# Performance work log

Measured on AMD Instinct MI355X. Metric: run time of the kernel, lower is better.

## Reference

```python
import jax, jax.numpy as jnp
import numpy as np

H, I, B = 256, 128, 512

def setup_inputs() -> dict:
    key = jax.random.key(0)
    ks = jax.random.split(key, 24)
    n = lambda k, shp, s=1.0: jax.random.normal(k, shp, dtype=jnp.float32) * s
    inp = {
        "x": n(ks[0], (B, I)),
        "hx": n(ks[1], (B, H), 0.1),
        "cx": n(ks[2], (B, H, H), 0.1),
        # input->gate weights (hidden, input), xavier-like scale
        "Wii": n(ks[3], (H, I), (2.0 / (H + I)) ** 0.5),
        "Wif": n(ks[4], (H, I), (2.0 / (H + I)) ** 0.5),
        "Wig": n(ks[5], (H, I), (2.0 / (H + I)) ** 0.5),
        "Wio": n(ks[6], (H, I), (2.0 / (H + I)) ** 0.5),
        # hidden->gate weights (hidden, hidden), ~orthogonal scale
        "Whi": n(ks[7], (H, H), H ** -0.5),
        "Whit": n(ks[8], (H, H), H ** -0.5),
        "Whf": n(ks[9], (H, H), H ** -0.5),
        "Whft": n(ks[10], (H, H), H ** -0.5),
        "Whc": n(ks[11], (H, H), H ** -0.5),
        "Whct": n(ks[12], (H, H), H ** -0.5),
        "Who": n(ks[13], (H, H), H ** -0.5),
        "Uinv": n(ks[14], (H, H), H ** -0.5),
        "Vtinv": n(ks[15], (H, H), H ** -0.5),
        # biases: bi/bf/bg are full (H,H) matrices, bo is (H,1)
        "bi": jnp.zeros((H, H), jnp.float32),
        "bf": jnp.zeros((H, H), jnp.float32),
        "bg": jnp.zeros((H, H), jnp.float32),
        "bo": jnp.zeros((H, 1), jnp.float32),
    }
    return inp


def reference(x, hx, cx, Wii, Wif, Wig, Wio, Whi, Whit, Whf, Whft, Whc, Whct, Who, Uinv, Vtinv, bi, bf, bg, bo):
    # W @ diag(v) @ M^T  ==  einsum('hi,bi,gi->bhg', W, v, M)
    def sandwich(Wx, Wh, Wht, b):
        # (Wx*x) @ Wx^T + (Wh*hx) @ Wht^T + b  -> (B,H,H)
        xt = jnp.einsum('hi,bi,gi->bhg', Wx, x, Wx)
        ht = jnp.einsum('hj,bj,gj->bhg', Wh, hx, Wht)
        return xt + ht + b

    i = jax.nn.sigmoid(sandwich(Wii, Whi, Whit, bi))
    f = jax.nn.sigmoid(sandwich(Wif, Whf, Whft, bf))
    g = jnp.tanh(sandwich(Wig, Whc, Whct, bg))
    # o: ordinary vector gate (B,H)
    o = jax.nn.sigmoid(jnp.einsum('hi,bi->bh', Wio, x)
                       + jnp.einsum('hj,bj->bh', Who, hx) + bo[:, 0])
    cx_new = f * cx + i * g                     # (B,H,H)
    # diag(Uinv @ cx_new @ Vtinv) per batch element -> (B,H)
    proj_down = jnp.einsum('ij,bjk,ki->bi', Uinv, cx_new, Vtinv)
    hx_new = o * jax.nn.sigmoid(proj_down)
    return hx_new
```

## Files before the change

kernel.cpp:

```cpp
#include <hip/hip_runtime.h>
#include <hip/hip_bf16.h>

#define Hh 256
#define Ii 128
#define KF 384
#define LDSB 72

typedef __attribute__((ext_vector_type(8))) short bf16x8;
typedef __attribute__((ext_vector_type(4))) float f32x4;
typedef unsigned short u16;
typedef unsigned int u32;

__device__ inline u16 f2bf(float f) {
  u32 u = __float_as_uint(f);
  u += 0x7FFFu + ((u >> 16) & 1u);
  return (u16)(u >> 16);
}
__device__ inline u32 pack_bf16x2(float a, float b) {
  __hip_bfloat162 h = __float22bfloat162_rn(make_float2(a, b));
  u32 r; __builtin_memcpy(&r, &h, 4); return r;
}
__device__ inline u32 scale2(u32 packed, float va, float vb) {
  float lo = __uint_as_float(packed << 16) * va;
  float hi = __uint_as_float(packed & 0xFFFF0000u) * vb;
  return pack_bf16x2(lo, hi);
}
__device__ inline float sigm(float x) { return 1.0f / (1.0f + __expf(-x)); }
__device__ inline float tanh_f(float x) { return 1.0f - 2.0f / (1.0f + __expf(2.0f * x)); }

union U32x4 { bf16x8 f; u32 d[4]; uint4 v; };

__global__ __launch_bounds__(256) void k_prep(
    const float* __restrict__ Wii, const float* __restrict__ Wif, const float* __restrict__ Wig,
    const float* __restrict__ Whi, const float* __restrict__ Whit,
    const float* __restrict__ Whf, const float* __restrict__ Whft,
    const float* __restrict__ Whc, const float* __restrict__ Whct,
    const float* __restrict__ Vtinv, const float* __restrict__ Uinv,
    const float* __restrict__ Wio, const float* __restrict__ Who,
    u16* __restrict__ RW, u16* __restrict__ CW, u16* __restrict__ Vtt,
    float* __restrict__ UinvP, float* __restrict__ proj, float* __restrict__ WoT) {
  const int tid = threadIdx.x, bx = blockIdx.x, y = blockIdx.y;
  if (y < 3) {
    if (bx < 48) {
      const float* WX  = (y == 0) ? Wii : (y == 1 ? Wif : Wig);
      const float* WHr = (y == 0) ? Whi : (y == 1 ? Whf : Whc);
      u16* rw = RW + y * Hh * KF;
      const int f  = (bx * 256 + tid) * 8;
      const int kc = f >> 14;
      const int h  = (f >> 6) & 255;
      const int t0 = f & 63;
      const float* src = (kc < 2) ? (WX + h * Ii + kc * 64 + t0)
                                  : (WHr + h * Hh + (kc - 2) * 64 + t0);
      const float4 s0 = *(const float4*)src;
      const float4 s1 = *(const float4*)(src + 4);
      uint4 o;
      o.x = (u32)f2bf(s0.x) | ((u32)f2bf(s0.y) << 16);
      o.y = (u32)f2bf(s0.z) | ((u32)f2bf(s0.w) << 16);
      o.z = (u32)f2bf(s1.x) | ((u32)f2bf(s1.y) << 16);
      o.w = (u32)f2bf(s1.z) | ((u32)f2bf(s1.w) << 16);
      *(uint4*)(rw + f) = o;
    }
  } else if (y < 6) {
    if (bx < 48) {
      const int ph = y - 3;
      const float* WX  = (ph == 0) ? Wii : (ph == 1 ? Wif : Wig);
      const float* WHt = (ph == 0) ? Whit : (ph == 1 ? Whft : Whct);
      u16* cw = CW + ph * Hh * KF;
      const int f  = (bx * 256 + tid) * 8;
      const int kb = f / 24576;
      const int r  = f - kb * 24576;
      const int kc = r >> 12;
      const int r2 = r & 4095;
      const int k  = r2 >> 6;
      const int t0 = r2 & 63;
      const int h  = kb * 64 + k;
      const float* src = (kc < 2) ? (WX + h * Ii + kc * 64 + t0)
                                  : (WHt + h * Hh + (kc - 2) * 64 + t0);
      const float4 s0 = *(const float4*)src;
      const float4 s1 = *(const float4*)(src + 4);
      uint4 o;
      o.x = (u32)f2bf(s0.x) | ((u32)f2bf(s0.y) << 16);
      o.y = (u32)f2bf(s0.z) | ((u32)f2bf(s0.w) << 16);
      o.z = (u32)f2bf(s1.x) | ((u32)f2bf(s1.y) << 16);
      o.w = (u32)f2bf(s1.z) | ((u32)f2bf(s1.w) << 16);
      *(uint4*)(cw + f) = o;
    }
  } else if (y == 6) {
    if (bx < 64) {
      __shared__ u16 tbuf[32][33];
      const int c = tid & 31, r8 = tid >> 5;
      const int tr = bx >> 3, tc = bx & 7;
#pragma unroll
      for (int rr = r8; rr < 32; rr += 8)
        tbuf[rr][c] = f2bf(Vtinv[(tc * 32 + rr) * Hh + tr * 32 + c]);
      __syncthreads();
#pragma unroll
      for (int rr = r8; rr < 32; rr += 8)
        Vtt[(tr * 32 + rr) * Hh + tc * 32 + c] = tbuf[c][rr];
    } else {
      const int tb = (bx - 64) * 12;
#pragma unroll
      for (int tt = 0; tt < 12; ++tt) {
        const int t = tb + tt;
        const float v = (t < Ii) ? Wio[tid * Ii + t] : Who[tid * Hh + t - Ii];
        WoT[t * Hh + tid] = v;
      }
    }
  } else {
    if (bx < 32) {
      const int base = (bx * 256 + tid) * 8;
#pragma unroll
      for (int e8 = 0; e8 < 8; ++e8) {
        int f = base + e8;
        int t512 = f >> 7;
        int e = f & 127;
        int ti = e >> 5;
        int rem = e & 31;
        int tjl = rem >> 2;
        int rr = rem & 3;
        int wv = t512 >> 6;
        int ln = t512 & 63;
        int qd = ln >> 4;
        int r15v = ln & 15;
        int i = (wv & 3) * 64 + ti * 16 + qd * 4 + rr;
        int j = (wv >> 2) * 128 + tjl * 16 + r15v;
        UinvP[f] = Uinv[i * Hh + j];
      }
    } else if (bx < 64) {
      const int base = (bx - 32) * 256 + tid;
      const float4 z = {0.f, 0.f, 0.f, 0.f};
#pragma unroll
      for (int it = 0; it < 4; ++it)
        *(float4*)(proj + (size_t)(it * 8192 + base) * 4) = z;
    }
  }
}

__global__ __launch_bounds__(512) void k_main(
    const float* __restrict__ x, const float* __restrict__ hx, const float* __restrict__ cx,
    const u16* __restrict__ RW, const u16* __restrict__ CW, const u16* __restrict__ Vtt,
    const float* __restrict__ bi, const float* __restrict__ bfm, const float* __restrict__ bg,
    const float* __restrict__ UinvP, float* __restrict__ proj) {
  __shared__ union {
    u16 B[2][64][LDSB];
    u16 P[256][LDSB];
  } sU;
  __shared__ float sV[KF];
  __shared__ float sPart[8][64];

  const int tid  = threadIdx.x;
  const int b    = blockIdx.x >> 2;
  const int kb   = blockIdx.x & 3;
  const int k0   = kb * 64;
  const int lane = tid & 63;
  const int w    = tid >> 6;
  const int r15  = lane & 15;
  const int quad = lane >> 4;

  if (tid < Ii) sV[tid] = x[b * Ii + tid];
  if (tid < Hh) sV[Ii + tid] = hx[b * Hh + tid];

  const u16* rwp[3] = {RW + 2 * Hh * KF, RW, RW + 1 * Hh * KF};
  const u16* cwp[3] = {CW + 2 * Hh * KF + kb * 24576, CW + kb * 24576,
                       CW + 1 * Hh * KF + kb * 24576};
  const float* bp3[2] = {bg, bi};
  const float* cx_b = cx + (size_t)b * Hh * Hh;

  const int wfoff = (w * 32 + r15) * 64 + quad * 8;

  U32x4 m, mnW, mnN;
  bf16x8 wfC[2][2], wfN[2][2];
  m.v   = *(const uint4*)(cwp[0] + tid * 8);
  mnW.v = *(const uint4*)(cwp[0] + 4096 + tid * 8);
  {
    const u16* rb = rwp[0] + wfoff;
#pragma unroll
    for (int ja = 0; ja < 2; ++ja)
#pragma unroll
      for (int ks = 0; ks < 2; ++ks)
        wfC[ja][ks] = *(const bf16x8*)(rb + ja * 1024 + ks * 32);
  }
  __syncthreads();
  {
    U32x4 o;
    const float4 va = *(const float4*)(&sV[(tid & 7) * 8]);
    const float4 vb = *(const float4*)(&sV[(tid & 7) * 8 + 4]);
    o.d[0] = scale2(m.d[0], va.x, va.y); o.d[1] = scale2(m.d[1], va.z, va.w);
    o.d[2] = scale2(m.d[2], vb.x, vb.y); o.d[3] = scale2(m.d[3], vb.z, vb.w);
    *(uint4*)(&sU.B[0][tid >> 3][(tid & 7) * 8]) = o.v;
  }
  __syncthreads();

  float p[2][4][4];
  f32x4 acc[2][4];

#pragma unroll
  for (int ph = 0; ph < 3; ++ph) {
#pragma unroll
    for (int ja = 0; ja < 2; ++ja)
#pragma unroll
      for (int tk = 0; tk < 4; ++tk)
#pragma unroll
        for (int r = 0; r < 4; ++r) acc[ja][tk][r] = 0.0f;

#pragma unroll
    for (int kc = 0; kc < 6; ++kc) {
      const int sc  = ph * 6 + kc;
      const int cur = sc & 1;
      if (sc < 16) {
        const int s2 = sc + 2;
        mnN.v = *(const uint4*)(cwp[s2 / 6] + (s2 % 6) * 4096 + tid * 8);
      }
      if (sc < 17) {
        const int s1 = sc + 1;
        const u16* rb = rwp[s1 / 6] + (s1 % 6) * 16384 + wfoff;
#pragma unroll
        for (int ja = 0; ja < 2; ++ja)
#pragma unroll
          for (int ks = 0; ks < 2; ++ks)
            wfN[ja][ks] = *(const bf16x8*)(rb + ja * 1024 + ks * 32);
      }
#pragma unroll
      for (int ks = 0; ks < 2; ++ks) {
        bf16x8 sf[4];
#pragma unroll
        for (int tk = 0; tk < 4; ++tk)
          sf[tk] = *(const bf16x8*)(&sU.B[cur][tk * 16 + r15][ks * 32 + quad * 8]);
#pragma unroll
        for (int tk = 0; tk < 4; ++tk) {
          acc[0][tk] = __builtin_amdgcn_mfma_f32_16x16x32_bf16(sf[tk], wfC[0][ks], acc[0][tk], 0, 0, 0);
          acc[1][tk] = __builtin_amdgcn_mfma_f32_16x16x32_bf16(sf[tk], wfC[1][ks], acc[1][tk], 0, 0, 0);
        }
      }
      if (sc < 17) {
        U32x4 o;
        const int nt0 = ((sc + 1) % 6) * 64;
        const float4 va = *(const float4*)(&sV[nt0 + (tid & 7) * 8]);
        const float4 vb = *(const float4*)(&sV[nt0 + (tid & 7) * 8 + 4]);
        o.d[0] = scale2(mnW.d[0], va.x, va.y); o.d[1] = scale2(mnW.d[1], va.z, va.w);
        o.d[2] = scale2(mnW.d[2], vb.x, vb.y); o.d[3] = scale2(mnW.d[3], vb.z, vb.w);
        *(uint4*)(&sU.B[cur ^ 1][tid >> 3][(tid & 7) * 8]) = o.v;
      }
      if (ph < 2 && kc == 5) {
        const float* bp = bp3[ph];
#pragma unroll
        for (int ja = 0; ja < 2; ++ja) {
          const int jg = w * 32 + ja * 16 + r15;
          const float* bpr = bp + (size_t)jg * Hh + k0 + quad * 4;
#pragma unroll
          for (int tk = 0; tk < 4; ++tk) {
            const float4 bv = *(const float4*)(bpr + tk * 16);
            if (ph == 0) {
#pragma unroll
              for (int r = 0; r < 4; ++r)
                p[ja][tk][r] = tanh_f(acc[ja][tk][r] + ((const float*)&bv)[r]);
            } else {
#pragma unroll
              for (int r = 0; r < 4; ++r)
                p[ja][tk][r] *= sigm(acc[ja][tk][r] + ((const float*)&bv)[r]);
            }
          }
        }
      }
      __syncthreads();
      mnW = mnN;
#pragma unroll
      for (int ja = 0; ja < 2; ++ja)
#pragma unroll
        for (int ks = 0; ks < 2; ++ks)
          wfC[ja][ks] = wfN[ja][ks];
    }
  }

#pragma unroll
  for (int ja = 0; ja < 2; ++ja) {
    const int jg = w * 32 + ja * 16 + r15;
    const float* bpr = bfm + (size_t)jg * Hh + k0 + quad * 4;
    const float* cxr = cx_b + (size_t)jg * Hh + k0 + quad * 4;
#pragma unroll
    for (int tk = 0; tk < 4; ++tk) {
      const float4 bv = *(const float4*)(bpr + tk * 16);
      const float4 cv = *(const float4*)(cxr + tk * 16);
      float cc[4];
#pragma unroll
      for (int r = 0; r < 4; ++r)
        cc[r] = sigm(acc[ja][tk][r] + ((const float*)&bv)[r]) * ((const float*)&cv)[r] + p[ja][tk][r];
      uint2 pk;
      pk.x = pack_bf16x2(cc[0], cc[1]);
      pk.y = pack_bf16x2(cc[2], cc[3]);
      *(uint2*)(&sU.P[jg][tk * 16 + quad * 4]) = pk;
    }
  }
  __syncthreads();

  const int islab = (w & 3) * 64;
  const int jhb   = (w >> 2) * 128;
  const float* up = UinvP + (size_t)tid * 128;
  float racc[4][4];
#pragma unroll
  for (int ti = 0; ti < 4; ++ti)
#pragma unroll
    for (int r = 0; r < 4; ++r) racc[ti][r] = 0.0f;

#pragma unroll
  for (int tjg = 0; tjg < 2; ++tjg) {
    bf16x8 fbp[2][4];
#pragma unroll
    for (int ks = 0; ks < 2; ++ks)
#pragma unroll
      for (int tjj = 0; tjj < 4; ++tjj)
        fbp[ks][tjj] = *(const bf16x8*)(&sU.P[jhb + (tjg * 4 + tjj) * 16 + r15][ks * 32 + quad * 8]);
#pragma unroll
    for (int ti = 0; ti < 4; ++ti) {
      const u16* vrow = Vtt + (size_t)(islab + ti * 16 + r15) * Hh + k0 + quad * 8;
      const bf16x8 va0 = *(const bf16x8*)vrow;
      const bf16x8 va1 = *(const bf16x8*)(vrow + 32);
      f32x4 pacc[4];
#pragma unroll
      for (int tjj = 0; tjj < 4; ++tjj)
#pragma unroll
        for (int r = 0; r < 4; ++r) pacc[tjj][r] = 0.0f;
#pragma unroll
      for (int tjj = 0; tjj < 4; ++tjj)
        pacc[tjj] = __builtin_amdgcn_mfma_f32_16x16x32_bf16(va0, fbp[0][tjj], pacc[tjj], 0, 0, 0);
#pragma unroll
      for (int tjj = 0; tjj < 4; ++tjj)
        pacc[tjj] = __builtin_amdgcn_mfma_f32_16x16x32_bf16(va1, fbp[1][tjj], pacc[tjj], 0, 0, 0);
#pragma unroll
      for (int tjj = 0; tjj < 4; ++tjj) {
        const float4 uu = *(const float4*)(up + ti * 32 + (tjg * 4 + tjj) * 4);
#pragma unroll
        for (int r = 0; r < 4; ++r)
          racc[ti][r] += pacc[tjj][r] * ((const float*)&uu)[r];
      }
    }
  }

#pragma unroll
  for (int ti = 0; ti < 4; ++ti)
#pragma unroll
    for (int r = 0; r < 4; ++r) {
      float v = racc[ti][r];
      v += __shfl_xor(v, 1);
      v += __shfl_xor(v, 2);
      v += __shfl_xor(v, 4);
      v += __shfl_xor(v, 8);
      if (r15 == 0) sPart[w][ti * 16 + quad * 4 + r] = v;
    }
  __syncthreads();
  if (tid < Hh)
    atomicAdd(&proj[b * Hh + tid], sPart[tid >> 6][tid & 63] + sPart[(tid >> 6) + 4][tid & 63]);
}

__global__ __launch_bounds__(256) void k_out(
    const float* __restrict__ x, const float* __restrict__ hx,
    const float* __restrict__ WoT, const float* __restrict__ bo,
    const float* __restrict__ proj, float* __restrict__ out) {
  __shared__ float sv[KF];
  const int b = blockIdx.x, tid = threadIdx.x;
  if (tid < Ii) sv[tid] = x[b * Ii + tid];
  sv[Ii + tid] = hx[b * Hh + tid];
  __syncthreads();
  float acc = 0.0f;
  const float* wp = WoT + tid;
#pragma unroll 16
  for (int t = 0; t < KF; ++t)
    acc = fmaf(sv[t], wp[(size_t)t * Hh], acc);
  out[b * Hh + tid] = sigm(acc + bo[tid]) * sigm(proj[b * Hh + tid]);
}

extern "C" void kernel_launch(void* const* d_in, const int* in_sizes, int n_in,
                              void* d_out, int out_size, void* d_ws, size_t ws_size,
                              hipStream_t stream) {
  (void)in_sizes; (void)n_in; (void)out_size; (void)ws_size;
  const float* x    = (const float*)d_in[0];
  const float* hx   = (const float*)d_in[1];
  const float* cx   = (const float*)d_in[2];
  const float* Wii  = (const float*)d_in[3];
  const float* Wif  = (const float*)d_in[4];
  const float* Wig  = (const float*)d_in[5];
  const float* Wio  = (const float*)d_in[6];
  const float* Whi  = (const float*)d_in[7];
  const float* Whit = (const float*)d_in[8];
  const float* Whf  = (const float*)d_in[9];
  const float* Whft = (const float*)d_in[10];
  const float* Whc  = (const float*)d_in[11];
  const float* Whct = (const float*)d_in[12];
  const float* Who  = (const float*)d_in[13];
  const float* Uinv = (const float*)d_in[14];
  const float* Vtinv= (const float*)d_in[15];
  const float* bi   = (const float*)d_in[16];
  const float* bf   = (const float*)d_in[17];
  const float* bg   = (const float*)d_in[18];
  const float* bo   = (const float*)d_in[19];
  float* out = (float*)d_out;

  u16* RW    = (u16*)d_ws;
  u16* CW    = RW + 3 * Hh * KF;
  u16* Vtt   = CW + 3 * Hh * KF;
  float* UinvP = (float*)(Vtt + Hh * Hh);
  float* proj  = UinvP + Hh * Hh;
  float* WoT   = proj + 512 * Hh;

  k_prep<<<dim3(96, 8), 256, 0, stream>>>(Wii, Wif, Wig, Whi, Whit, Whf, Whft, Whc, Whct,
                                          Vtinv, Uinv, Wio, Who,
                                          RW, CW, Vtt, UinvP, proj, WoT);
  k_main<<<2048, 512, 0, stream>>>(x, hx, cx, RW, CW, Vtt, bi, bf, bg, UinvP, proj);
  k_out<<<512, 256, 0, stream>>>(x, hx, WoT, bo, proj, out);
}
```

Baseline: 521.6 us.

## Stage full per-phase operand tile in LDS to cut per-chunk barriers

Replaces the double-buffered 64-wide LDS chunk pipeline, which synced after every k-chunk, with a single 64x384 LDS tile that holds a whole phase's scaled operand. Barriers drop from one per chunk to two per phase, and the next phase's global loads are issued mid-phase into registers. Weight-fragment loads are no longer prefetched one step ahead, so global latency may be exposed before each chunk's MFMAs. More registers (six uint4) and more LDS are used, which could lower occupancy.

```diff
diff --git a/kernel.cpp b/kernel.cpp
--- a/kernel.cpp
+++ b/kernel.cpp
@@ -5,6 +5,7 @@
 #define Ii 128
 #define KF 384
 #define LDSB 72
+#define SBN 392
 
 typedef __attribute__((ext_vector_type(8))) short bf16x8;
 typedef __attribute__((ext_vector_type(4))) float f32x4;
@@ -142,7 +143,7 @@
     const float* __restrict__ bi, const float* __restrict__ bfm, const float* __restrict__ bg,
     const float* __restrict__ UinvP, float* __restrict__ proj) {
   __shared__ union {
-    u16 B[2][64][LDSB];
+    u16 B[64][SBN];
     u16 P[256][LDSB];
   } sU;
   __shared__ float sV[KF];
@@ -156,6 +157,8 @@
   const int w    = tid >> 6;
   const int r15  = lane & 15;
   const int quad = lane >> 4;
+  const int srow = tid >> 3;
+  const int scol = (tid & 7) * 8;
 
   if (tid < Ii) sV[tid] = x[b * Ii + tid];
   if (tid < Hh) sV[Ii + tid] = hx[b * Hh + tid];
@@ -168,26 +171,19 @@
 
   const int wfoff = (w * 32 + r15) * 64 + quad * 8;
 
-  U32x4 m, mnW, mnN;
-  bf16x8 wfC[2][2], wfN[2][2];
-  m.v   = *(const uint4*)(cwp[0] + tid * 8);
-  mnW.v = *(const uint4*)(cwp[0] + 4096 + tid * 8);
-  {
-    const u16* rb = rwp[0] + wfoff;
-#pragma unroll
-    for (int ja = 0; ja < 2; ++ja)
-#pragma unroll
-      for (int ks = 0; ks < 2; ++ks)
-        wfC[ja][ks] = *(const bf16x8*)(rb + ja * 1024 + ks * 32);
-  }
-  __syncthreads();
-  {
+  U32x4 L[6];
+#pragma unroll
+  for (int kc = 0; kc < 6; ++kc)
+    L[kc].v = *(const uint4*)(cwp[0] + kc * 4096 + tid * 8);
+  __syncthreads();
+#pragma unroll
+  for (int kc = 0; kc < 6; ++kc) {
     U32x4 o;
-    const float4 va = *(const float4*)(&sV[(tid & 7) * 8]);
-    const float4 vb = *(const float4*)(&sV[(tid & 7) * 8 + 4]);
-    o.d[0] = scale2(m.d[0], va.x, va.y); o.d[1] = scale2(m.d[1], va.z, va.w);
-    o.d[2] = scale2(m.d[2], vb.x, vb.y); o.d[3] = scale2(m.d[3], vb.z, vb.w);
-    *(uint4*)(&sU.B[0][tid >> 3][(tid & 7) * 8]) = o.v;
+    const float4 va = *(const float4*)(&sV[kc * 64 + scol]);
+    const float4 vb = *(const float4*)(&sV[kc * 64 + scol + 4]);
+    o.d[0] = scale2(L[kc].d[0], va.x, va.y); o.d[1] = scale2(L[kc].d[1], va.z, va.w);
+    o.d[2] = scale2(L[kc].d[2], vb.x, vb.y); o.d[3] = scale2(L[kc].d[3], vb.z, vb.w);
+    *(uint4*)(&sU.B[srow][kc * 64 + scol]) = o.v;
   }
   __syncthreads();
 
@@ -205,73 +201,69 @@
 
 #pragma unroll
     for (int kc = 0; kc < 6; ++kc) {
-      const int sc  = ph * 6 + kc;
-      const int cur = sc & 1;
-      if (sc < 16) {
-        const int s2 = sc + 2;
-        mnN.v = *(const uint4*)(cwp[s2 / 6] + (s2 % 6) * 4096 + tid * 8);
-      }
-      if (sc < 17) {
-        const int s1 = sc + 1;
-        const u16* rb = rwp[s1 / 6] + (s1 % 6) * 16384 + wfoff;
+      if (ph < 2 && kc == 3) {
+#pragma unroll
+        for (int k2 = 0; k2 < 6; ++k2)
+          L[k2].v = *(const uint4*)(cwp[ph + 1] + k2 * 4096 + tid * 8);
+      }
+      bf16x8 wf[2][2];
+      {
+        const u16* rb = rwp[ph] + kc * 16384 + wfoff;
 #pragma unroll
         for (int ja = 0; ja < 2; ++ja)
 #pragma unroll
           for (int ks = 0; ks < 2; ++ks)
-            wfN[ja][ks] = *(const bf16x8*)(rb + ja * 1024 + ks * 32);
+            wf[ja][ks] = *(const bf16x8*)(rb + ja * 1024 + ks * 32);
       }
 #pragma unroll
       for (int ks = 0; ks < 2; ++ks) {
         bf16x8 sf[4];
 #pragma unroll
         for (int tk = 0; tk < 4; ++tk)
-          sf[tk] = *(const bf16x8*)(&sU.B[cur][tk * 16 + r15][ks * 32 + quad * 8]);
+          sf[tk] = *(const bf16x8*)(&sU.B[tk * 16 + r15][kc * 64 + ks * 32 + quad * 8]);
 #pragma unroll
         for (int tk = 0; tk < 4; ++tk) {
-          acc[0][tk] = __builtin_amdgcn_mfma_f32_16x16x32_bf16(sf[tk], wfC[0][ks], acc[0][tk], 0, 0, 0);
-          acc[1][tk] = __builtin_amdgcn_mfma_f32_16x16x32_bf16(sf[tk], wfC[1][ks], acc[1][tk], 0, 0, 0);
+          acc[0][tk] = __builtin_amdgcn_mfma_f32_16x16x32_bf16(sf[tk], wf[0][ks], acc[0][tk], 0, 0, 0);
+          acc[1][tk] = __builtin_amdgcn_mfma_f32_16x16x32_bf16(sf[tk], wf[1][ks], acc[1][tk], 0, 0, 0);
         }
       }
-      if (sc < 17) {
-        U32x4 o;
-        const int nt0 = ((sc + 1) % 6) * 64;
-        const float4 va = *(const float4*)(&sV[nt0 + (tid & 7) * 8]);
-        const float4 vb = *(const float4*)(&sV[nt0 + (tid & 7) * 8 + 4]);
-        o.d[0] = scale2(mnW.d[0], va.x, va.y); o.d[1] = scale2(mnW.d[1], va.z, va.w);
-        o.d[2] = scale2(mnW.d[2], vb.x, vb.y); o.d[3] = scale2(mnW.d[3], vb.z, vb.w);
-        *(uint4*)(&sU.B[cur ^ 1][tid >> 3][(tid & 7) * 8]) = o.v;
-      }
-      if (ph < 2 && kc == 5) {
-        const float* bp = bp3[ph];
-#pragma unroll
-        for (int ja = 0; ja < 2; ++ja) {
-          const int jg = w * 32 + ja * 16 + r15;
-          const float* bpr = bp + (size_t)jg * Hh + k0 + quad * 4;
-#pragma unroll
-          for (int tk = 0; tk < 4; ++tk) {
-            const float4 bv = *(const float4*)(bpr + tk * 16);
-            if (ph == 0) {
-#pragma unroll
-              for (int r = 0; r < 4; ++r)
-                p[ja][tk][r] = tanh_f(acc[ja][tk][r] + ((const float*)&bv)[r]);
-            } else {
-#pragma unroll
-              for (int r = 0; r < 4; ++r)
-                p[ja][tk][r] *= sigm(acc[ja][tk][r] + ((const float*)&bv)[r]);
-            }
+    }
+
+    if (ph < 2) {
+      const float* bp = bp3[ph];
+#pragma unroll
+      for (int ja = 0; ja < 2; ++ja) {
+        const int jg = w * 32 + ja * 16 + r15;
+        const float* bpr = bp + (size_t)jg * Hh + k0 + quad * 4;
+#pragma unroll
+        for (int tk = 0; tk < 4; ++tk) {
+          const float4 bv = *(const float4*)(bpr + tk * 16);
+          if (ph == 0) {
+#pragma unroll
+            for (int r = 0; r < 4; ++r)
+              p[ja][tk][r] = tanh_f(acc[ja][tk][r] + ((const float*)&bv)[r]);
+          } else {
+#pragma unroll
+            for (int r = 0; r < 4; ++r)
+              p[ja][tk][r] *= sigm(acc[ja][tk][r] + ((const float*)&bv)[r]);
           }
         }
       }
       __syncthreads();
-      mnW = mnN;
-#pragma unroll
-      for (int ja = 0; ja < 2; ++ja)
-#pragma unroll
-        for (int ks = 0; ks < 2; ++ks)
-          wfC[ja][ks] = wfN[ja][ks];
+#pragma unroll
+      for (int kc = 0; kc < 6; ++kc) {
+        U32x4 o;
+        const float4 va = *(const float4*)(&sV[kc * 64 + scol]);
+        const float4 vb = *(const float4*)(&sV[kc * 64 + scol + 4]);
+        o.d[0] = scale2(L[kc].d[0], va.x, va.y); o.d[1] = scale2(L[kc].d[1], va.z, va.w);
+        o.d[2] = scale2(L[kc].d[2], vb.x, vb.y); o.d[3] = scale2(L[kc].d[3], vb.z, vb.w);
+        *(uint4*)(&sU.B[srow][kc * 64 + scol]) = o.v;
+      }
+      __syncthreads();
     }
   }
 
+  __syncthreads();
 #pragma unroll
   for (int ja = 0; ja < 2; ++ja) {
     const int jg = w * 32 + ja * 16 + r15;
```

Result: slower. 536.3 us (+2.8%).
